# Optimization experiments

Measured on AMD Instinct MI355X. Metric: run time of the kernel, lower is better.

Reference implementation:

```python
import jax, jax.numpy as jnp
import numpy as np

M0, M1 = 16, 8          # scalar / vector multiplicities (16x0e + 8x1o)
NB = 16                  # number_of_basis
RMAX = 8.0               # max_radius
N_NODES, N_EDGES = 10000, 160000
WNUM = M0*M0 + M0*M1 + M1*M1 + M1*M0  # 576, tp weight_numel


def sus(t):
    """e3nn soft_unit_step: exp(-1/t) for t>0 else 0."""
    safe = jnp.where(t > 0, t, 1.0)
    return jnp.where(t > 0, jnp.exp(-1.0 / safe), 0.0)


def setup_inputs():
    key = jax.random.key(0)
    ks = jax.random.split(key, 12)
    D = M0 + 3 * M1  # 40
    x = jax.random.normal(ks[0], (N_NODES, D), jnp.float32)
    edge_index = jax.random.randint(ks[1], (2, N_EDGES), 0, N_NODES, jnp.int32)
    edge_attr = jax.random.normal(ks[2], (N_EDGES, 4), jnp.float32)  # sh lmax=1
    node_attr = jnp.ones((N_NODES, 1), jnp.float32)
    batch = jnp.zeros((N_NODES,), jnp.int32)
    amf = jax.random.uniform(ks[3], (N_EDGES, 1), jnp.float32) * RMAX  # edge lengths
    Wq0 = jax.random.normal(ks[4], (M0, M0), jnp.float32)
    Wq1 = jax.random.normal(ks[5], (M1, M1), jnp.float32)
    Wk1 = jax.random.normal(ks[6], (NB, 16), jnp.float32)
    Wk2 = jax.random.normal(ks[7], (16, WNUM), jnp.float32)
    Wv1 = jax.random.normal(ks[8], (NB, 16), jnp.float32)
    Wv2 = jax.random.normal(ks[9], (16, WNUM), jnp.float32)
    Wd0 = jax.random.normal(ks[10], (M0, M0), jnp.float32)
    Wd1 = jax.random.normal(ks[11], (M1, M1), jnp.float32)
    return dict(x=x, edge_index=edge_index, edge_attr=edge_attr, node_attr=node_attr,
                batch=batch, additional_message_features=amf,
                Wq0=Wq0, Wq1=Wq1, Wk1=Wk1, Wk2=Wk2, Wv1=Wv1, Wv2=Wv2, Wd0=Wd0, Wd1=Wd1)


def reference(x, edge_index, edge_attr, node_attr, batch, additional_message_features,
              Wq0, Wq1, Wk1, Wk2, Wv1, Wv2, Wd0, Wd1):
    n = x.shape[0]
    src, dst = edge_index[0], edge_index[1]
    d = additional_message_features.reshape(-1)  # [E]

    # soft_one_hot_linspace(basis='smooth_finite', cutoff=True) * sqrt(NB)
    centers = jnp.linspace(0.0, RMAX, NB + 2)[1:-1]
    step = RMAX / (NB + 1)
    diff = (d[:, None] - centers) / step
    emb = (1.14136 * np.exp(2.0)) * sus(diff + 1.0) * sus(1.0 - diff) * np.sqrt(NB)  # [E,NB]
    cutoff = sus(10.0 * (1.0 - d / RMAX))  # [E]

    # split irreps: scalars [*,M0], vectors [*,M1,3]
    x0 = x[:, :M0]
    x1 = x[:, M0:].reshape(n, M1, 3)

    # q = Linear(input_irreps -> hidden_irreps): per-irrep linear, 1/sqrt(fan_in)
    q0 = (x0 @ Wq0) / np.sqrt(M0)
    q1 = jnp.einsum('nui,uw->nwi', x1, Wq1) / np.sqrt(M1)

    # radial MLPs producing per-edge tensor-product weights
    def radial(W1, W2):
        h = jax.nn.silu((emb @ W1) / np.sqrt(NB))
        return (h @ W2) / np.sqrt(16.0)  # [E, WNUM]
    wk = radial(Wk1, Wk2)
    wv = radial(Wv1, Wv2)

    xs0, xs1 = x0[src], x1[src]           # gather by edge source
    sh0, sh1 = edge_attr[:, 0], edge_attr[:, 1:4]
    dot11 = jnp.einsum('eui,ei->eu', xs1, sh1) / np.sqrt(3.0)  # 1o x 1o -> 0e CG

    def fctp(w):
        # FullyConnectedTensorProduct(input, sh, out) with per-edge weights.
        s1 = M0 * M0
        s2 = s1 + M0 * M1
        s3 = s2 + M1 * M1
        w1 = w[:, :s1].reshape(-1, M0, M0)   # 0e x 0e -> 0e
        w2 = w[:, s1:s2].reshape(-1, M0, M1) # 0e x 1o -> 1o
        w3 = w[:, s2:s3].reshape(-1, M1, M1) # 1o x 0e -> 1o
        w4 = w[:, s3:].reshape(-1, M1, M0)   # 1o x 1o -> 0e
        norm = 1.0 / np.sqrt(M0 + M1)        # path fan-in normalization
        o0 = (jnp.einsum('euw,eu->ew', w1, xs0 * sh0[:, None]) +
              jnp.einsum('euw,eu->ew', w4, dot11)) * norm            # [E,M0]
        o1 = (jnp.einsum('euw,eu,ei->ewi', w2, xs0, sh1) +
              jnp.einsum('euw,eui->ewi', w3, xs1 * sh0[:, None, None])) * norm  # [E,M1,3]
        return o0, o1

    k0, k1 = fctp(wk)
    v0, v1 = fctp(wv)

    # dot: FullyConnectedTensorProduct(hidden, hidden, '0e') with shared weights
    score = (jnp.einsum('eu,ev,uv->e', q0[dst], k0, Wd0) +
             jnp.einsum('eui,evi,uv->e', q1[dst], k1, Wd1) / np.sqrt(3.0)) / np.sqrt(M0*M0 + M1*M1)

    expv = cutoff * jnp.exp(score)                                   # [E]
    z = jax.ops.segment_sum(expv, dst, num_segments=n)               # [N]
    z = jnp.where(z == 0, 1.0, z)
    alpha = expv / z[dst]
    we = jnp.sqrt(jax.nn.relu(alpha))                                # alpha.relu().sqrt()
    v = jnp.concatenate([v0, v1.reshape(-1, 3 * M1)], axis=1)        # [E,40]
    return jax.ops.segment_sum(we[:, None] * v, dst, num_segments=n) # [N,40]
```

## Files before the change

### kernel.cpp

```cpp
#include <hip/hip_runtime.h>
#include <hip/hip_bf16.h>

#define E_CNT 160000
#define N_CNT 10000

#define INV_STEP   2.125f
#define EMB_C      33.734292f
#define INVS320    0.05590170f
#define INVS8      0.35355339f
#define INV_SQRT3  0.57735027f
#define KSCALE     0.051031036f

#define OFF_FLAG   0
#define OFF_EAF    400016
#define OFF_AMFF   1040016
#define OFF_WK1F   1200656
#define OFF_WV1F   1200912
#define OFF_P      1219600
#define OFF_EXPV   1619600
#define OFF_VBUF   1779600
#define OFF_DEG    8179600
#define OFF_Z      8179600
#define OFF_DEG2   8189600
#define OFF_START  8199600
#define OFF_START2 8209601
#define OFF_CURS   8219602
#define OFF_CURS2  8229602
#define OFF_DPOS   8239602
#define OFF_ELIST2 8399602
#define OFF_G      8559632


static __device__ __forceinline__ float bf2f(__hip_bfloat16 b) { return __bfloat162float(b); }
static __device__ __forceinline__ float sanitize(float v) {
    return fminf(fmaxf(v, -1e30f), 1e30f);
}
static __device__ __forceinline__ unsigned short f2bf(float f) {
    unsigned x = __float_as_uint(f);
    unsigned r = (x + 0x7fffu + ((x >> 16) & 1u)) >> 16;
    return (unsigned short)r;
}
static __device__ __forceinline__ float bflo(unsigned u) { return __uint_as_float(u << 16); }
static __device__ __forceinline__ float bfhi(unsigned u) { return __uint_as_float(u & 0xffff0000u); }
static __device__ __forceinline__ float2 bfp(unsigned u) {
    float2 r; r.x = bflo(u); r.y = bfhi(u); return r;
}

static __device__ __forceinline__ float dot2bf(unsigned a, unsigned b, float c)
{
    float d;
    asm("v_dot2_f32_bf16 %0, %1, %2, %3" : "=v"(d) : "v"(a), "v"(b), "v"(c));
    return d;
}
static __device__ __forceinline__ unsigned cvtpk2(float lo, float hi)
{
    unsigned r;
    asm("v_cvt_pk_bf16_f32 %0, %1, %2" : "=v"(r) : "v"(lo), "v"(hi));
    return r;
}
static __device__ __forceinline__ void splitpk(float a0, float a1, unsigned& ph, unsigned& pl)
{
    ph = cvtpk2(a0, a1);
    pl = cvtpk2(a0 - bflo(ph), a1 - bfhi(ph));
}

static __device__ __forceinline__ float4 load4(const void* p, int i4, int f32)
{
    if (f32) return ((const float4*)p)[i4];
    uint2 u = ((const uint2*)p)[i4];
    float4 r;
    r.x = bflo(u.x); r.y = bfhi(u.x);
    r.z = bflo(u.y); r.w = bfhi(u.y);
    return r;
}

static __device__ __forceinline__ void ld8(const float* p, float (&r)[8])
{
    float4 a = ((const float4*)p)[0];
    float4 b = ((const float4*)p)[1];
    r[0] = a.x; r[1] = a.y; r[2] = a.z; r[3] = a.w;
    r[4] = b.x; r[5] = b.y; r[6] = b.z; r[7] = b.w;
}
static __device__ __forceinline__ void ld8(const __hip_bfloat16* p, float (&r)[8])
{
    uint4 u = *(const uint4*)p;
    r[0] = bflo(u.x); r[1] = bfhi(u.x); r[2] = bflo(u.y); r[3] = bfhi(u.y);
    r[4] = bflo(u.z); r[5] = bfhi(u.z); r[6] = bflo(u.w); r[7] = bfhi(u.w);
}

__global__ __launch_bounds__(256) void init_kernel(
    const unsigned short* __restrict__ xb, float* __restrict__ ws)
{
    const int idx = blockIdx.x * 256 + threadIdx.x;
    if (idx < 20000) ((int*)(ws + OFF_DEG))[idx] = 0;
    if (blockIdx.x == 0 && threadIdx.x < 64) {
        const int lane = threadIdx.x;
        unsigned e0 = (unsigned)((xb[2 * lane] >> 7) & 0xFF);
        unsigned e1 = (unsigned)((xb[128 + 2 * lane] >> 7) & 0xFF);
        int c = (e0 >= 141 ? 1 : 0) + (e1 >= 141 ? 1 : 0);
#pragma unroll
        for (int off = 1; off < 64; off <<= 1) c += __shfl_xor(c, off);
        if (lane == 0) *(int*)ws = (c >= 8) ? 1 : 0;
    }
}

static __device__ __forceinline__ void do_prep(
    const void* __restrict__ ea, const void* __restrict__ amf,
    const void* __restrict__ Wk1, const void* __restrict__ Wv1,
    const int* __restrict__ ei, float* __restrict__ ws, int i, int f32)
{
    if (i < 160000) ((float4*)(ws + OFF_EAF))[i] = load4(ea, i, f32);
    if (i < 40000) {
        ((float4*)(ws + OFF_AMFF))[i] = load4(amf, i, f32);
#pragma unroll
        for (int k = 0; k < 4; ++k) {
            atomicAdd((int*)(ws + OFF_DEG)  + ei[E_CNT + 4 * i + k], 1);
            atomicAdd((int*)(ws + OFF_DEG2) + ei[4 * i + k], 1);
        }
    }
    if (i < 64) {
        ((float4*)(ws + OFF_WK1F))[i] = load4(Wk1, i, f32);
        ((float4*)(ws + OFF_WV1F))[i] = load4(Wv1, i, f32);
    }
}

template <typename T>
static __device__ __forceinline__ void build_G(
    const T* __restrict__ x, const T* __restrict__ W2b, int n, int p, int c, int u,
    float* __restrict__ ws)
{
    float xs[40];
#pragma unroll
    for (int q = 0; q < 5; ++q) ld8(x + n * 40 + q * 8, *(float(*)[8])(xs + q * 8));
    const T* W2 = W2b + c * 576;

    float out[96];
#pragma unroll
    for (int k = 0; k < 96; ++k) out[k] = 0.f;

#pragma unroll
    for (int uu = 0; uu < 16; ++uu) {
        float r0[8], r1[8];
        ld8(W2 + uu * 16, r0);
        ld8(W2 + uu * 16 + 8, r1);
        const float xv = xs[uu];
#pragma unroll
        for (int w = 0; w < 8; ++w) {
            out[w]     = fmaf(r0[w], xv, out[w]);
            out[8 + w] = fmaf(r1[w], xv, out[8 + w]);
        }
    }
#pragma unroll
    for (int uu = 0; uu < 16; ++uu) {
        float r[8];
        ld8(W2 + 256 + uu * 8, r);
        const float xv = xs[uu];
#pragma unroll
        for (int w = 0; w < 8; ++w) out[16 + w] = fmaf(r[w], xv, out[16 + w]);
    }
#pragma unroll
    for (int uu = 0; uu < 8; ++uu) {
        float r[8];
        ld8(W2 + 384 + uu * 8, r);
        const float a0 = xs[16 + uu * 3 + 0];
        const float a1 = xs[16 + uu * 3 + 1];
        const float a2 = xs[16 + uu * 3 + 2];
#pragma unroll
        for (int w = 0; w < 8; ++w) {
            out[24 + w * 3 + 0] = fmaf(r[w], a0, out[24 + w * 3 + 0]);
            out[24 + w * 3 + 1] = fmaf(r[w], a1, out[24 + w * 3 + 1]);
            out[24 + w * 3 + 2] = fmaf(r[w], a2, out[24 + w * 3 + 2]);
        }
    }
#pragma unroll
    for (int uu = 0; uu < 8; ++uu) {
        float r0[8], r1[8];
        ld8(W2 + 448 + uu * 16, r0);
        ld8(W2 + 448 + uu * 16 + 8, r1);
        const float a0 = xs[16 + uu * 3 + 0];
        const float a1 = xs[16 + uu * 3 + 1];
        const float a2 = xs[16 + uu * 3 + 2];
#pragma unroll
        for (int w = 0; w < 8; ++w) {
            out[48 + w * 3 + 0] = fmaf(r0[w], a0, out[48 + w * 3 + 0]);
            out[48 + w * 3 + 1] = fmaf(r0[w], a1, out[48 + w * 3 + 1]);
            out[48 + w * 3 + 2] = fmaf(r0[w], a2, out[48 + w * 3 + 2]);
            out[48 + (8 + w) * 3 + 0] = fmaf(r1[w], a0, out[48 + (8 + w) * 3 + 0]);
            out[48 + (8 + w) * 3 + 1] = fmaf(r1[w], a1, out[48 + (8 + w) * 3 + 1]);
            out[48 + (8 + w) * 3 + 2] = fmaf(r1[w], a2, out[48 + (8 + w) * 3 + 2]);
        }
    }
#pragma unroll
    for (int k = 0; k < 48; ++k) out[48 + k] *= INV_SQRT3;

    uint4 ov[12];
    unsigned* ou = (unsigned*)ov;
#pragma unroll
    for (int kk = 0; kk < 48; ++kk) {
        float oa = __shfl_xor(out[kk], 1);
        float ob = __shfl_xor(out[48 + kk], 1);
        float lov = u ? ob : out[kk];
        float hiv = u ? out[48 + kk] : oa;
        ou[kk] = (unsigned)f2bf(lov) | ((unsigned)f2bf(hiv) << 16);
    }
    const int jj = (c >> 1) & 7;
    uint4* gb = (uint4*)(ws + OFF_G)
              + ((size_t)(p * 8 + jj) * 10000 + n) * 24 + u * 12;
#pragma unroll
    for (int q = 0; q < 12; ++q) gb[q] = ov[q];
}

template <typename T>
static __device__ __forceinline__ void build_P(
    const T* __restrict__ x, const T* __restrict__ Wq0, const T* __restrict__ Wq1,
    const T* __restrict__ Wd0, const T* __restrict__ Wd1, int n, float* __restrict__ ws)
{
    float xs[40];
#pragma unroll
    for (int q = 0; q < 5; ++q) ld8(x + n * 40 + q * 8, *(float(*)[8])(xs + q * 8));

    float q0[16];
#pragma unroll
    for (int w = 0; w < 16; ++w) q0[w] = 0.f;
#pragma unroll
    for (int u = 0; u < 16; ++u) {
        float r0[8], r1[8];
        ld8(Wq0 + u * 16, r0);
        ld8(Wq0 + u * 16 + 8, r1);
        const float xv = xs[u];
#pragma unroll
        for (int w = 0; w < 8; ++w) {
            q0[w]     = fmaf(r0[w], xv, q0[w]);
            q0[8 + w] = fmaf(r1[w], xv, q0[8 + w]);
        }
    }
#pragma unroll
    for (int w = 0; w < 16; ++w) q0[w] *= 0.25f;

    float p0[16];
#pragma unroll
    for (int v = 0; v < 16; ++v) p0[v] = 0.f;
#pragma unroll
    for (int w = 0; w < 16; ++w) {
        float r0[8], r1[8];
        ld8(Wd0 + w * 16, r0);
        ld8(Wd0 + w * 16 + 8, r1);
        const float qv = q0[w];
#pragma unroll
        for (int v = 0; v < 8; ++v) {
            p0[v]     = fmaf(r0[v], qv, p0[v]);
            p0[8 + v] = fmaf(r1[v], qv, p0[8 + v]);
        }
    }
    float* pn = ws + OFF_P + n * 40;
#pragma unroll
    for (int v = 0; v < 16; ++v) pn[v] = sanitize(p0[v] * INVS320);

    float q1[24];
#pragma unroll
    for (int k = 0; k < 24; ++k) q1[k] = 0.f;
#pragma unroll
    for (int u = 0; u < 8; ++u) {
        float r[8];
        ld8(Wq1 + u * 8, r);
        const float a0 = xs[16 + u * 3 + 0];
        const float a1 = xs[16 + u * 3 + 1];
        const float a2 = xs[16 + u * 3 + 2];
#pragma unroll
        for (int w = 0; w < 8; ++w) {
            q1[w * 3 + 0] = fmaf(r[w], a0, q1[w * 3 + 0]);
            q1[w * 3 + 1] = fmaf(r[w], a1, q1[w * 3 + 1]);
            q1[w * 3 + 2] = fmaf(r[w], a2, q1[w * 3 + 2]);
        }
    }
#pragma unroll
    for (int k = 0; k < 24; ++k) q1[k] *= INVS8;

    float p1[24];
#pragma unroll
    for (int k = 0; k < 24; ++k) p1[k] = 0.f;
#pragma unroll
    for (int w = 0; w < 8; ++w) {
        float r[8];
        ld8(Wd1 + w * 8, r);
        const float b0 = q1[w * 3 + 0];
        const float b1 = q1[w * 3 + 1];
        const float b2 = q1[w * 3 + 2];
#pragma unroll
        for (int v = 0; v < 8; ++v) {
            p1[v * 3 + 0] = fmaf(r[v], b0, p1[v * 3 + 0]);
            p1[v * 3 + 1] = fmaf(r[v], b1, p1[v * 3 + 1]);
            p1[v * 3 + 2] = fmaf(r[v], b2, p1[v * 3 + 2]);
        }
    }
    const float sc = INVS320 * INV_SQRT3;
#pragma unroll
    for (int k = 0; k < 24; ++k) pn[16 + k] = sanitize(p1[k] * sc);
}

__global__ __launch_bounds__(256) void gp_kernel(
    const void* __restrict__ x,
    const void* __restrict__ Wq0, const void* __restrict__ Wq1,
    const void* __restrict__ Wk2, const void* __restrict__ Wv2,
    const void* __restrict__ Wd0, const void* __restrict__ Wd1,
    const void* __restrict__ ea, const void* __restrict__ amf,
    const void* __restrict__ Wk1, const void* __restrict__ Wv1,
    const int* __restrict__ ei,
    float* __restrict__ ws)
{
    const int f32 = *(const int*)ws;
    const int tid = threadIdx.x;
    const int blk = blockIdx.x;
    if (blk < 625) {
        do_prep(ea, amf, Wk1, Wv1, ei, ws, blk * 256 + tid, f32);
        return;
    }
    if (blk < 1875) {
        const int t  = (blk - 625) * 256 + tid;
        const int j2 = t / 20000;
        const int r  = t - j2 * 20000;
        const int n  = r >> 1;
        const int u  = r & 1;
        const int p  = j2 >> 3;
        const int jj = j2 & 7;
        const int c  = jj * 2 + u;
        const void* W2b = p ? Wv2 : Wk2;
        if (f32) build_G((const float*)x, (const float*)W2b, n, p, c, u, ws);
        else     build_G((const __hip_bfloat16*)x, (const __hip_bfloat16*)W2b, n, p, c, u, ws);
        return;
    }
    {
        const int n = (blk - 1875) * 256 + tid;
        if (n >= N_CNT) return;
        if (f32) build_P((const float*)x, (const float*)Wq0, (const float*)Wq1,
                         (const float*)Wd0, (const float*)Wd1, n, ws);
        else     build_P((const __hip_bfloat16*)x, (const __hip_bfloat16*)Wq0,
                         (const __hip_bfloat16*)Wq1, (const __hip_bfloat16*)Wd0,
                         (const __hip_bfloat16*)Wd1, n, ws);
    }
}

__global__ __launch_bounds__(512) void scan_kernel(float* __restrict__ ws)
{
    __shared__ int ssum[512];
    const int t    = threadIdx.x;
    const int half = t >> 8;
    const int lt   = t & 255;
    int* deg   = (int*)(ws + (half ? OFF_DEG2   : OFF_DEG));
    int* start = (int*)(ws + (half ? OFF_START2 : OFF_START));
    int* curs  = (int*)(ws + (half ? OFF_CURS2  : OFF_CURS));
    const int base = lt * 40;
    int s = 0;
    for (int k = 0; k < 40; ++k) {
        int idx = base + k;
        if (idx < N_CNT) s += deg[idx];
    }
    ssum[t] = s;
    __syncthreads();
    for (int off = 1; off < 256; off <<= 1) {
        int v = (lt >= off) ? ssum[t - off] : 0;
        __syncthreads();
        ssum[t] += v;
        __syncthreads();
    }
    int run = ssum[t] - s;
    for (int k = 0; k < 40; ++k) {
        int idx = base + k;
        if (idx < N_CNT) {
            start[idx] = run;
            curs[idx]  = run;
            run += deg[idx];
        }
    }
    if (lt == 255) start[N_CNT] = E_CNT;
    __syncthreads();
    for (int k = t; k < N_CNT; k += 512) ws[OFF_Z + k] = 0.f;
}

__global__ __launch_bounds__(256) void fill_kernel(const int* __restrict__ ei, float* __restrict__ ws)
{
    const int e = blockIdx.x * 256 + threadIdx.x;
    int pd = atomicAdd((int*)(ws + OFF_CURS)  + ei[E_CNT + e], 1);
    int ps = atomicAdd((int*)(ws + OFF_CURS2) + ei[e], 1);
    ((int*)(ws + OFF_ELIST2))[ps] = e;
    ((int*)(ws + OFF_DPOS))[ps]   = pd;
}

static __device__ __forceinline__ void load12c(unsigned (&ub)[48], const uint4* __restrict__ p0)
{
#pragma unroll
    for (int q = 0; q < 12; ++q) {
        uint4 v = p0[q];
        ub[4 * q + 0] = v.x; ub[4 * q + 1] = v.y;
        ub[4 * q + 2] = v.z; ub[4 * q + 3] = v.w;
    }
}

static __device__ __forceinline__ void accum_lo(const unsigned (&ub)[48],
    float h0, float h1, float sh0,
    float (&o0)[16], float (&o1)[24], float (&t2a)[8])
{
    unsigned hsH, hsL, hcH, hcL;
    splitpk(h0 * sh0, h1 * sh0, hsH, hsL);
    splitpk(h0, h1, hcH, hcL);
#pragma unroll
    for (int w = 0; w < 16; ++w)
        o0[w] = dot2bf(ub[w], hsL, dot2bf(ub[w], hsH, o0[w]));
#pragma unroll
    for (int w = 0; w < 8; ++w)
        t2a[w] = dot2bf(ub[16 + w], hcL, dot2bf(ub[16 + w], hcH, t2a[w]));
#pragma unroll
    for (int k = 0; k < 24; ++k)
        o1[k] = dot2bf(ub[24 + k], hsL, dot2bf(ub[24 + k], hsH, o1[k]));
}
static __device__ __forceinline__ void accum_hi(const unsigned (&ub)[48],
    float h0, float h1, float s1x, float s1y, float s1z, float (&o0)[16])
{
    unsigned hxH, hxL, hyH, hyL, hzH, hzL;
    splitpk(h0 * s1x, h1 * s1x, hxH, hxL);
    splitpk(h0 * s1y, h1 * s1y, hyH, hyL);
    splitpk(h0 * s1z, h1 * s1z, hzH, hzL);
#pragma unroll
    for (int w = 0; w < 16; ++w) {
        float acc = o0[w];
        acc = dot2bf(ub[3 * w + 0], hxL, dot2bf(ub[3 * w + 0], hxH, acc));
        acc = dot2bf(ub[3 * w + 1], hyL, dot2bf(ub[3 * w + 1], hyH, acc));
        acc = dot2bf(ub[3 * w + 2], hzL, dot2bf(ub[3 * w + 2], hzH, acc));
        o0[w] = acc;
    }
}

__global__ __launch_bounds__(128) void edge_kernel(
    const int* __restrict__ ei, float* __restrict__ ws)
{
    const int tid  = threadIdx.x;
    const int pass = tid >> 6;
    const int lane = tid & 63;
    const int b  = blockIdx.x;
    const int lb = (b < 2496) ? ((b & 7) * 312 + (b >> 3)) : b;
    const int sidx = lb * 64 + lane;
    const int e    = ((const int*)(ws + OFF_ELIST2))[sidx];
    const int dpos = ((const int*)(ws + OFF_DPOS))[sidx];
    const int src  = ei[e];
    const int dst  = ei[E_CNT + e];

    const uint4* gb = (const uint4*)(ws + OFF_G) + ((size_t)pass * 80000 + src) * 24;
    unsigned A[48], B[48];
    load12c(A, gb);
    load12c(B, gb + 12);

    const float d   = ws[OFF_AMFF + e];
    const float dsv = d * INV_STEP;
    const int i1 = (int)ceilf(dsv) - 1;
    const int i0 = i1 - 1;
    float e0 = 0.f, e1 = 0.f;
    {
        float t1 = dsv - (float)i0;
        float t2 = (float)(i0 + 2) - dsv;
        if (i0 >= 0 && i0 <= 15 && t2 > 0.f)
            e0 = EMB_C * expf(-1.f / t1 - 1.f / t2);
        float u1 = dsv - (float)i1;
        float u2 = (float)(i1 + 2) - dsv;
        if (i1 >= 0 && i1 <= 15 && u1 > 0.f)
            e1 = EMB_C * expf(-1.f / u1 - 1.f / u2);
    }
    const int r0i = (i0 < 0 ? 0 : (i0 > 15 ? 15 : i0)) << 4;
    const int r1i = (i1 < 0 ? 0 : (i1 > 15 ? 15 : i1)) << 4;

    const float* W1 = ws + (pass ? OFF_WV1F : OFF_WK1F);
    float h[16];
#pragma unroll
    for (int j = 0; j < 16; ++j) {
        float s = fmaf(e1, W1[r1i + j], e0 * W1[r0i + j]);
        s *= 0.25f;
        h[j] = s / (1.f + expf(-s));
    }

    const float4 eav = ((const float4*)(ws + OFF_EAF))[e];
    const float sh0 = eav.x, s1x = eav.y, s1y = eav.z, s1z = eav.w;

    float o0[16], o1[24], t2a[8];
#pragma unroll
    for (int i = 0; i < 16; ++i) o0[i] = 0.f;
#pragma unroll
    for (int i = 0; i < 24; ++i) o1[i] = 0.f;
#pragma unroll
    for (int i = 0; i < 8; ++i) t2a[i] = 0.f;

#pragma unroll
    for (int s = 0; s < 16; s += 2) {
        const int jj = s >> 1;
        accum_lo(A, h[2 * jj], h[2 * jj + 1], sh0, o0, o1, t2a);
        if (s + 2 < 16) load12c(A, gb + (size_t)(jj + 1) * 240000);
        accum_hi(B, h[2 * jj], h[2 * jj + 1], s1x, s1y, s1z, o0);
        if (s + 3 < 16) load12c(B, gb + (size_t)(jj + 1) * 240000 + 12);
    }

#pragma unroll
    for (int w = 0; w < 8; ++w) {
        o1[w * 3 + 0] = fmaf(t2a[w], s1x, o1[w * 3 + 0]);
        o1[w * 3 + 1] = fmaf(t2a[w], s1y, o1[w * 3 + 1]);
        o1[w * 3 + 2] = fmaf(t2a[w], s1z, o1[w * 3 + 2]);
    }

    if (pass == 0) {
        const float* pd = ws + OFF_P + dst * 40;
        float sc = 0.f;
#pragma unroll
        for (int j = 0; j < 16; ++j) sc = fmaf(o0[j], pd[j], sc);
#pragma unroll
        for (int j = 0; j < 24; ++j) sc = fmaf(o1[j], pd[16 + j], sc);
        sc = fminf(fmaxf(sc * KSCALE, -60.f), 60.f);
        float ct = 10.f * (1.f - d * 0.125f);
        float cutoff = (ct > 0.f) ? expf(-1.f / ct) : 0.f;
        float ev = fmaxf(cutoff * expf(sc), 0.f);
        ws[OFF_EXPV + dpos] = ev;
        atomicAdd(ws + OFF_Z + dst, ev);
    } else {
        float vo[40];
#pragma unroll
        for (int j = 0; j < 16; ++j) vo[j] = sanitize(o0[j] * KSCALE);
#pragma unroll
        for (int j = 0; j < 24; ++j) vo[16 + j] = sanitize(o1[j] * KSCALE);
        uint4 pk[5];
        unsigned* pu = (unsigned*)pk;
#pragma unroll
        for (int k = 0; k < 20; ++k)
            pu[k] = (unsigned)f2bf(vo[2 * k]) | ((unsigned)f2bf(vo[2 * k + 1]) << 16);
        uint4* vr = (uint4*)((unsigned short*)(ws + OFF_VBUF) + (size_t)dpos * 40);
#pragma unroll
        for (int q = 0; q < 5; ++q) vr[q] = pk[q];
    }
}

__global__ __launch_bounds__(256) void gather_kernel(
    const float* __restrict__ ws, void* __restrict__ out)
{
    const int i = blockIdx.x * 256 + threadIdx.x;
    if (i >= N_CNT * 10) return;
    const int n = i / 10;
    const int q = i - n * 10;
    const int* start = (const int*)(ws + OFF_START);
    const float* expv = ws + OFF_EXPV;
    const unsigned* Vb = (const unsigned*)(ws + OFF_VBUF);
    const int s = start[n], t = start[n + 1];

    float zz = ws[OFF_Z + n];
    const float rz = (zz > 0.f) ? 1.f / zz : 1.f;

    float ax = 0.f, ay = 0.f, az = 0.f, aw = 0.f;
    for (int j = s; j < t; ++j) {
        const float we = sqrtf(fmaxf(expv[j] * rz, 0.f));
        uint2 u = *(const uint2*)(Vb + (size_t)j * 20 + 2 * q);
        float2 v0 = bfp(u.x), v1 = bfp(u.y);
        ax = fmaf(we, v0.x, ax); ay = fmaf(we, v0.y, ay);
        az = fmaf(we, v1.x, az); aw = fmaf(we, v1.y, aw);
    }
    ax = sanitize(ax); ay = sanitize(ay); az = sanitize(az); aw = sanitize(aw);
    const int f32 = *(const int*)ws;
    if (f32) {
        float4 o; o.x = ax; o.y = ay; o.z = az; o.w = aw;
        ((float4*)out)[(size_t)n * 10 + q] = o;
    } else {
        uint2 o;
        o.x = (unsigned)f2bf(ax) | ((unsigned)f2bf(ay) << 16);
        o.y = (unsigned)f2bf(az) | ((unsigned)f2bf(aw) << 16);
        ((uint2*)out)[(size_t)n * 10 + q] = o;
    }
}

extern "C" void kernel_launch(void* const* d_in, const int* in_sizes, int n_in,
                              void* d_out, int out_size, void* d_ws, size_t ws_size,
                              hipStream_t stream)
{
    (void)in_sizes; (void)n_in; (void)out_size; (void)ws_size;
    const void* x   = d_in[0];
    const int*  ei  = (const int*)d_in[1];
    const void* ea  = d_in[2];
    const void* amf = d_in[5];
    const void* Wq0 = d_in[6];
    const void* Wq1 = d_in[7];
    const void* Wk1 = d_in[8];
    const void* Wk2 = d_in[9];
    const void* Wv1 = d_in[10];
    const void* Wv2 = d_in[11];
    const void* Wd0 = d_in[12];
    const void* Wd1 = d_in[13];

    float* ws = (float*)d_ws;

    init_kernel<<<79, 256, 0, stream>>>((const unsigned short*)x, ws);
    gp_kernel<<<1915, 256, 0, stream>>>(x, Wq0, Wq1, Wk2, Wv2, Wd0, Wd1,
                                        ea, amf, Wk1, Wv1, (const int*)ei, ws);
    scan_kernel<<<1, 512, 0, stream>>>(ws);
    fill_kernel<<<625, 256, 0, stream>>>(ei, ws);
    edge_kernel<<<2500, 128, 0, stream>>>(ei, ws);
    gather_kernel<<<(N_CNT * 10 + 255) / 256, 256, 0, stream>>>(ws, d_out);
}
```

Before: 293.5 us.

## Store G buffer plane-major and stream per-chunk stores in builder

```diff
diff --git a/kernel.cpp b/kernel.cpp
--- a/kernel.cpp
+++ b/kernel.cpp
@@ -88,6 +88,24 @@
     r[4] = bflo(u.z); r[5] = bfhi(u.z); r[6] = bflo(u.w); r[7] = bfhi(u.w);
 }
 
+#define PSQ(gs, kq, a0, a1, a2, a3, u, ustore)                                 \
+    do {                                                                       \
+        float v0_ = __shfl_xor((a0), 1), v1_ = __shfl_xor((a1), 1);            \
+        float v2_ = __shfl_xor((a2), 1), v3_ = __shfl_xor((a3), 1);            \
+        if ((u) == (ustore)) {                                                 \
+            float l0_ = (u) ? v0_ : (a0), h0_ = (u) ? (a0) : v0_;              \
+            float l1_ = (u) ? v1_ : (a1), h1_ = (u) ? (a1) : v1_;              \
+            float l2_ = (u) ? v2_ : (a2), h2_ = (u) ? (a2) : v2_;              \
+            float l3_ = (u) ? v3_ : (a3), h3_ = (u) ? (a3) : v3_;              \
+            uint4 t_;                                                          \
+            t_.x = (unsigned)f2bf(l0_) | ((unsigned)f2bf(h0_) << 16);          \
+            t_.y = (unsigned)f2bf(l1_) | ((unsigned)f2bf(h1_) << 16);          \
+            t_.z = (unsigned)f2bf(l2_) | ((unsigned)f2bf(h2_) << 16);          \
+            t_.w = (unsigned)f2bf(l3_) | ((unsigned)f2bf(h3_) << 16);          \
+            (gs)[(size_t)(kq) * 10000] = t_;                                   \
+        }                                                                      \
+    } while (0)
+
 __global__ __launch_bounds__(256) void init_kernel(
     const unsigned short* __restrict__ xb, float* __restrict__ ws)
 {
@@ -133,81 +151,106 @@
 #pragma unroll
     for (int q = 0; q < 5; ++q) ld8(x + n * 40 + q * 8, *(float(*)[8])(xs + q * 8));
     const T* W2 = W2b + c * 576;
-
-    float out[96];
-#pragma unroll
-    for (int k = 0; k < 96; ++k) out[k] = 0.f;
-
-#pragma unroll
-    for (int uu = 0; uu < 16; ++uu) {
-        float r0[8], r1[8];
-        ld8(W2 + uu * 16, r0);
-        ld8(W2 + uu * 16 + 8, r1);
-        const float xv = xs[uu];
-#pragma unroll
-        for (int w = 0; w < 8; ++w) {
-            out[w]     = fmaf(r0[w], xv, out[w]);
-            out[8 + w] = fmaf(r1[w], xv, out[8 + w]);
-        }
-    }
-#pragma unroll
-    for (int uu = 0; uu < 16; ++uu) {
-        float r[8];
-        ld8(W2 + 256 + uu * 8, r);
-        const float xv = xs[uu];
-#pragma unroll
-        for (int w = 0; w < 8; ++w) out[16 + w] = fmaf(r[w], xv, out[16 + w]);
-    }
-#pragma unroll
-    for (int uu = 0; uu < 8; ++uu) {
-        float r[8];
-        ld8(W2 + 384 + uu * 8, r);
-        const float a0 = xs[16 + uu * 3 + 0];
-        const float a1 = xs[16 + uu * 3 + 1];
-        const float a2 = xs[16 + uu * 3 + 2];
-#pragma unroll
-        for (int w = 0; w < 8; ++w) {
-            out[24 + w * 3 + 0] = fmaf(r[w], a0, out[24 + w * 3 + 0]);
-            out[24 + w * 3 + 1] = fmaf(r[w], a1, out[24 + w * 3 + 1]);
-            out[24 + w * 3 + 2] = fmaf(r[w], a2, out[24 + w * 3 + 2]);
-        }
-    }
-#pragma unroll
-    for (int uu = 0; uu < 8; ++uu) {
-        float r0[8], r1[8];
-        ld8(W2 + 448 + uu * 16, r0);
-        ld8(W2 + 448 + uu * 16 + 8, r1);
-        const float a0 = xs[16 + uu * 3 + 0];
-        const float a1 = xs[16 + uu * 3 + 1];
-        const float a2 = xs[16 + uu * 3 + 2];
-#pragma unroll
-        for (int w = 0; w < 8; ++w) {
-            out[48 + w * 3 + 0] = fmaf(r0[w], a0, out[48 + w * 3 + 0]);
-            out[48 + w * 3 + 1] = fmaf(r0[w], a1, out[48 + w * 3 + 1]);
-            out[48 + w * 3 + 2] = fmaf(r0[w], a2, out[48 + w * 3 + 2]);
-            out[48 + (8 + w) * 3 + 0] = fmaf(r1[w], a0, out[48 + (8 + w) * 3 + 0]);
-            out[48 + (8 + w) * 3 + 1] = fmaf(r1[w], a1, out[48 + (8 + w) * 3 + 1]);
-            out[48 + (8 + w) * 3 + 2] = fmaf(r1[w], a2, out[48 + (8 + w) * 3 + 2]);
-        }
-    }
-#pragma unroll
-    for (int k = 0; k < 48; ++k) out[48 + k] *= INV_SQRT3;
-
-    uint4 ov[12];
-    unsigned* ou = (unsigned*)ov;
-#pragma unroll
-    for (int kk = 0; kk < 48; ++kk) {
-        float oa = __shfl_xor(out[kk], 1);
-        float ob = __shfl_xor(out[48 + kk], 1);
-        float lov = u ? ob : out[kk];
-        float hiv = u ? out[48 + kk] : oa;
-        ou[kk] = (unsigned)f2bf(lov) | ((unsigned)f2bf(hiv) << 16);
-    }
-    const int jj = (c >> 1) & 7;
-    uint4* gb = (uint4*)(ws + OFF_G)
-              + ((size_t)(p * 8 + jj) * 10000 + n) * 24 + u * 12;
-#pragma unroll
-    for (int q = 0; q < 12; ++q) gb[q] = ov[q];
+    uint4* gs = (uint4*)(ws + OFF_G) + (size_t)(p * 8 + (c >> 1)) * 240000 + n;
+
+    {
+        float o[16];
+#pragma unroll
+        for (int k = 0; k < 16; ++k) o[k] = 0.f;
+#pragma unroll
+        for (int uu = 0; uu < 16; ++uu) {
+            float r0[8], r1[8];
+            ld8(W2 + uu * 16, r0);
+            ld8(W2 + uu * 16 + 8, r1);
+            const float xv = xs[uu];
+#pragma unroll
+            for (int w = 0; w < 8; ++w) {
+                o[w]     = fmaf(r0[w], xv, o[w]);
+                o[8 + w] = fmaf(r1[w], xv, o[8 + w]);
+            }
+        }
+        PSQ(gs, 0, o[0],  o[1],  o[2],  o[3],  u, 0);
+        PSQ(gs, 1, o[4],  o[5],  o[6],  o[7],  u, 0);
+        PSQ(gs, 2, o[8],  o[9],  o[10], o[11], u, 0);
+        PSQ(gs, 3, o[12], o[13], o[14], o[15], u, 0);
+    }
+    {
+        float o[8];
+#pragma unroll
+        for (int k = 0; k < 8; ++k) o[k] = 0.f;
+#pragma unroll
+        for (int uu = 0; uu < 16; ++uu) {
+            float r[8];
+            ld8(W2 + 256 + uu * 8, r);
+            const float xv = xs[uu];
+#pragma unroll
+            for (int w = 0; w < 8; ++w) o[w] = fmaf(r[w], xv, o[w]);
+        }
+        PSQ(gs, 4, o[0], o[1], o[2], o[3], u, 0);
+        PSQ(gs, 5, o[4], o[5], o[6], o[7], u, 0);
+    }
+    {
+        float o[24];
+#pragma unroll
+        for (int k = 0; k < 24; ++k) o[k] = 0.f;
+#pragma unroll
+        for (int uu = 0; uu < 8; ++uu) {
+            float r[8];
+            ld8(W2 + 384 + uu * 8, r);
+            const float a0 = xs[16 + uu * 3 + 0];
+            const float a1 = xs[16 + uu * 3 + 1];
+            const float a2 = xs[16 + uu * 3 + 2];
+#pragma unroll
+            for (int w = 0; w < 8; ++w) {
+                o[w * 3 + 0] = fmaf(r[w], a0, o[w * 3 + 0]);
+                o[w * 3 + 1] = fmaf(r[w], a1, o[w * 3 + 1]);
+                o[w * 3 + 2] = fmaf(r[w], a2, o[w * 3 + 2]);
+            }
+        }
+        PSQ(gs, 6,  o[0],  o[1],  o[2],  o[3],  u, 0);
+        PSQ(gs, 7,  o[4],  o[5],  o[6],  o[7],  u, 0);
+        PSQ(gs, 8,  o[8],  o[9],  o[10], o[11], u, 0);
+        PSQ(gs, 9,  o[12], o[13], o[14], o[15], u, 0);
+        PSQ(gs, 10, o[16], o[17], o[18], o[19], u, 0);
+        PSQ(gs, 11, o[20], o[21], o[22], o[23], u, 0);
+    }
+    {
+        float o[48];
+#pragma unroll
+        for (int k = 0; k < 48; ++k) o[k] = 0.f;
+#pragma unroll
+        for (int uu = 0; uu < 8; ++uu) {
+            float r0[8], r1[8];
+            ld8(W2 + 448 + uu * 16, r0);
+            ld8(W2 + 448 + uu * 16 + 8, r1);
+            const float a0 = xs[16 + uu * 3 + 0];
+            const float a1 = xs[16 + uu * 3 + 1];
+            const float a2 = xs[16 + uu * 3 + 2];
+#pragma unroll
+            for (int w = 0; w < 8; ++w) {
+                o[w * 3 + 0] = fmaf(r0[w], a0, o[w * 3 + 0]);
+                o[w * 3 + 1] = fmaf(r0[w], a1, o[w * 3 + 1]);
+                o[w * 3 + 2] = fmaf(r0[w], a2, o[w * 3 + 2]);
+                o[(8 + w) * 3 + 0] = fmaf(r1[w], a0, o[(8 + w) * 3 + 0]);
+                o[(8 + w) * 3 + 1] = fmaf(r1[w], a1, o[(8 + w) * 3 + 1]);
+                o[(8 + w) * 3 + 2] = fmaf(r1[w], a2, o[(8 + w) * 3 + 2]);
+            }
+        }
+#pragma unroll
+        for (int k = 0; k < 48; ++k) o[k] *= INV_SQRT3;
+        PSQ(gs, 12, o[0],  o[1],  o[2],  o[3],  u, 1);
+        PSQ(gs, 13, o[4],  o[5],  o[6],  o[7],  u, 1);
+        PSQ(gs, 14, o[8],  o[9],  o[10], o[11], u, 1);
+        PSQ(gs, 15, o[12], o[13], o[14], o[15], u, 1);
+        PSQ(gs, 16, o[16], o[17], o[18], o[19], u, 1);
+        PSQ(gs, 17, o[20], o[21], o[22], o[23], u, 1);
+        PSQ(gs, 18, o[24], o[25], o[26], o[27], u, 1);
+        PSQ(gs, 19, o[28], o[29], o[30], o[31], u, 1);
+        PSQ(gs, 20, o[32], o[33], o[34], o[35], u, 1);
+        PSQ(gs, 21, o[36], o[37], o[38], o[39], u, 1);
+        PSQ(gs, 22, o[40], o[41], o[42], o[43], u, 1);
+        PSQ(gs, 23, o[44], o[45], o[46], o[47], u, 1);
+    }
 }
 
 template <typename T>
@@ -322,8 +365,7 @@
         const int n  = r >> 1;
         const int u  = r & 1;
         const int p  = j2 >> 3;
-        const int jj = j2 & 7;
-        const int c  = jj * 2 + u;
+        const int c  = (j2 & 7) * 2 + u;
         const void* W2b = p ? Wv2 : Wk2;
         if (f32) build_G((const float*)x, (const float*)W2b, n, p, c, u, ws);
         else     build_G((const __hip_bfloat16*)x, (const __hip_bfloat16*)W2b, n, p, c, u, ws);
@@ -386,11 +428,11 @@
     ((int*)(ws + OFF_DPOS))[ps]   = pd;
 }
 
-static __device__ __forceinline__ void load12c(unsigned (&ub)[48], const uint4* __restrict__ p0)
+static __device__ __forceinline__ void load48p(unsigned (&ub)[48], const uint4* __restrict__ p0)
 {
 #pragma unroll
     for (int q = 0; q < 12; ++q) {
-        uint4 v = p0[q];
+        uint4 v = p0[(size_t)q * 10000];
         ub[4 * q + 0] = v.x; ub[4 * q + 1] = v.y;
         ub[4 * q + 2] = v.z; ub[4 * q + 3] = v.w;
     }
@@ -444,10 +486,10 @@
     const int src  = ei[e];
     const int dst  = ei[E_CNT + e];
 
-    const uint4* gb = (const uint4*)(ws + OFF_G) + ((size_t)pass * 80000 + src) * 24;
+    const uint4* gb = (const uint4*)(ws + OFF_G) + (size_t)pass * 1920000 + src;
     unsigned A[48], B[48];
-    load12c(A, gb);
-    load12c(B, gb + 12);
+    load48p(A, gb);
+    load48p(B, gb + 120000);
 
     const float d   = ws[OFF_AMFF + e];
     const float dsv = d * INV_STEP;
@@ -488,12 +530,11 @@
     for (int i = 0; i < 8; ++i) t2a[i] = 0.f;
 
 #pragma unroll
-    for (int s = 0; s < 16; s += 2) {
-        const int jj = s >> 1;
+    for (int jj = 0; jj < 8; ++jj) {
         accum_lo(A, h[2 * jj], h[2 * jj + 1], sh0, o0, o1, t2a);
-        if (s + 2 < 16) load12c(A, gb + (size_t)(jj + 1) * 240000);
+        if (jj + 1 < 8) load48p(A, gb + (size_t)(jj + 1) * 240000);
         accum_hi(B, h[2 * jj], h[2 * jj + 1], s1x, s1y, s1z, o0);
-        if (s + 3 < 16) load12c(B, gb + (size_t)(jj + 1) * 240000 + 12);
+        if (jj + 1 < 8) load48p(B, gb + (size_t)(jj + 1) * 240000 + 120000);
     }
 
 #pragma unroll
```

New measurement: 291.8 us. About the same (-0.6%).
